# Performance work log

Measured on AMD Instinct MI355X. Metric: run time of the kernel, lower is better.

Reference implementation:

```python
import jax, jax.numpy as jnp
import numpy as np

B, T, H = 65536, 34, 64
T10_LO, T10_HI = 0.1, 5.0
M0_LO, M0_HI = 0.0, 10000.0


def setup_inputs() -> dict:
    key = jax.random.key(0)
    ks = jax.random.split(key, 24)
    sig = jax.random.uniform(ks[0], (B, T), jnp.float32, 0.1, 1.0)
    keep = jax.random.uniform(ks[1], (B, T)) > 0.3
    X_fa_in = jnp.where(keep, sig, 0.0)
    fa_vals = jax.random.uniform(ks[2], (B, T), jnp.float32, 0.05, 0.6)  # flip angles (rad)
    fa_mask = keep
    fa_len = jnp.sum(keep, axis=1).astype(jnp.int64)
    TR_vals = jax.random.uniform(ks[3], (B, 1), jnp.float32, 0.003, 0.01)
    gi = 1.0 / np.sqrt(H)
    p = {}
    p['gru_Wih'] = jax.random.uniform(ks[4], (3 * H, 2), jnp.float32, -gi, gi)
    p['gru_Whh'] = jax.random.uniform(ks[5], (3 * H, H), jnp.float32, -gi, gi)
    p['gru_bih'] = jax.random.uniform(ks[6], (3 * H,), jnp.float32, -gi, gi)
    p['gru_bhh'] = jax.random.uniform(ks[7], (3 * H,), jnp.float32, -gi, gi)
    p['score_T10_w'] = jax.random.normal(ks[8], (H,), jnp.float32) * gi
    p['score_M0_w'] = jax.random.normal(ks[9], (H,), jnp.float32) * gi
    def lin(kw, kb, fan_out, fan_in):
        b = 1.0 / np.sqrt(fan_in)
        return (jax.random.uniform(kw, (fan_out, fan_in), jnp.float32, -b, b),
                jax.random.uniform(kb, (fan_out,), jnp.float32, -b, b))
    p['regT_W1'], p['regT_b1'] = lin(ks[10], ks[11], 200, H)
    p['regT_W2'], p['regT_b2'] = lin(ks[12], ks[13], 200, 200)
    p['regT_W3'], p['regT_b3'] = lin(ks[14], ks[15], 1, 200)
    p['regM_W1'], p['regM_b1'] = lin(ks[16], ks[17], 200, H)
    p['regM_W2'], p['regM_b2'] = lin(ks[18], ks[19], 200, 200)
    p['regM_W3'], p['regM_b3'] = lin(ks[20], ks[21], 1, 200)
    return dict(X_fa_in=X_fa_in, fa_vals=fa_vals, fa_mask=fa_mask, fa_len=fa_len,
                TR_vals=TR_vals, **p)


def _forward_fill(X_fa_in, fa_vals):
    # Segmented last-observation-carried-forward via cummax of valid indices.
    valid = X_fa_in != 0
    idx = jnp.where(valid, jnp.arange(T)[None, :], -1)
    last = jax.lax.cummax(idx, axis=1)                     # [B,T] index of last nonzero
    g = jnp.clip(last, 0, T - 1)
    Xf = jnp.where(last >= 0, jnp.take_along_axis(X_fa_in, g, axis=1), 0.0)
    ff = jnp.where(last >= 0, jnp.take_along_axis(fa_vals, g, axis=1), 0.0)
    return Xf, ff


def _gru(x, Wih, Whh, bih, bhh):
    # x: [B,T,2] -> out: [B,T,H]; PyTorch GRU gate order (r, z, n)
    x_proj = jnp.einsum('btf,gf->btg', x, Wih) + bih       # [B,T,3H]
    def step(h, xp):
        gh = h @ Whh.T + bhh                               # [B,3H]
        xr, xz, xn = jnp.split(xp, 3, axis=-1)
        hr, hz, hn = jnp.split(gh, 3, axis=-1)
        r = jax.nn.sigmoid(xr + hr)
        z = jax.nn.sigmoid(xz + hz)
        n = jnp.tanh(xn + r * hn)
        h_new = (1.0 - z) * n + z * h
        return h_new, h_new
    h0 = jnp.zeros((x.shape[0], Whh.shape[1]), x.dtype)
    _, out = jax.lax.scan(step, h0, jnp.swapaxes(x_proj, 0, 1))
    return jnp.swapaxes(out, 0, 1)


def _mlp(h, W1, b1, W2, b2, W3, b3):
    # Dropout layers are identity in eval mode
    h = jax.nn.elu(h @ W1.T + b1)
    h = jax.nn.elu(h @ W2.T + b2)
    return h @ W3.T + b3


def reference(X_fa_in, fa_vals, fa_mask, fa_len, TR_vals,
              gru_Wih, gru_Whh, gru_bih, gru_bhh,
              score_T10_w, score_M0_w,
              regT_W1, regT_b1, regT_W2, regT_b2, regT_W3, regT_b3,
              regM_W1, regM_b1, regM_W2, regM_b2, regM_W3, regM_b3):
    Xf, ff = _forward_fill(X_fa_in, fa_vals)
    x = jnp.stack([Xf, ff], axis=-1)                       # [B,T,2]
    out = _gru(x, gru_Wih, gru_Whh, gru_bih, gru_bhh)      # [B,T,H]
    # attention pooling: softmax over time of a linear score
    sT = jax.nn.softmax(out @ score_T10_w, axis=1)[..., None]
    sM = jax.nn.softmax(out @ score_M0_w, axis=1)[..., None]
    hT = jnp.sum(out * sT, axis=1)                         # [B,H]
    hM = jnp.sum(out * sM, axis=1)
    T10_raw = _mlp(hT, regT_W1, regT_b1, regT_W2, regT_b2, regT_W3, regT_b3)[:, 0]
    M0_raw = _mlp(hM, regM_W1, regM_b1, regM_W2, regM_b2, regM_W3, regM_b3)[:, 0]
    T10 = T10_LO + jax.nn.sigmoid(T10_raw)[:, None] * (T10_HI - T10_LO)  # [B,1]
    M0 = M0_LO + jax.nn.sigmoid(M0_raw)[:, None] * (M0_HI - M0_LO)       # [B,1]
    R1 = 1.0 / T10
    E = jnp.exp(-TR_vals * R1)                             # [B,1]
    X_out = (1.0 - E) * jnp.sin(fa_vals) / (1.0 - jnp.cos(fa_vals) * E)  # [B,T]
    X_out = X_out * M0
    return (X_out, T10, M0)
```

## Files before the change

### kernel.cpp

```cpp
#include <hip/hip_runtime.h>

#define B_TOT 65536
#define T_LEN 34
#define HD 64
#define LOG2E 1.44269504088896340736f

typedef __attribute__((ext_vector_type(8))) short short8b;
typedef __attribute__((ext_vector_type(4))) short short4b;
typedef __attribute__((ext_vector_type(4))) float f32x4;
typedef __attribute__((ext_vector_type(4))) unsigned int u32x4;

__device__ __forceinline__ float frcp(float x){ return __builtin_amdgcn_rcpf(x); }
__device__ __forceinline__ float fexp2(float x){ return __builtin_amdgcn_exp2f(x); }
__device__ __forceinline__ float fsigmoid(float x){ return frcp(1.0f+__expf(-x)); }
__device__ __forceinline__ float felu(float x){ return x>0.0f ? x : (__expf(x)-1.0f); }

__device__ __forceinline__ unsigned short f2bf_rne(float f){
    unsigned int u = __float_as_uint(f);
    u += 0x7FFFu + ((u >> 16) & 1u);
    return (unsigned short)(u >> 16);
}
__device__ __forceinline__ float bf2f(unsigned short h){
    return __uint_as_float(((unsigned int)h) << 16);
}
__device__ __forceinline__ void split8(const float4& a, const float4& b,
                                       short8b& hi, short8b& lo){
    float f[8] = {a.x,a.y,a.z,a.w,b.x,b.y,b.z,b.w};
    #pragma unroll
    for (int i = 0; i < 8; ++i){
        unsigned short h = f2bf_rne(f[i]);
        hi[i] = (short)h;
        lo[i] = (short)f2bf_rne(f[i] - bf2f(h));
    }
}
__device__ __forceinline__ unsigned int cvt_pk_bf16(float lo, float hi){
    unsigned int r;
    asm("v_cvt_pk_bf16_f32 %0, %1, %2" : "=v"(r) : "v"(lo), "v"(hi));
    return r;
}
__device__ __forceinline__ int hswz(int r){ return ((r ^ (r >> 3)) & 7); }

__global__ __launch_bounds__(256)
void gru_attn_mfma(const float* __restrict__ Xin, const float* __restrict__ FA,
                   const float* __restrict__ Wih, const float* __restrict__ Whh,
                   const float* __restrict__ bih, const float* __restrict__ bhh,
                   const float* __restrict__ swT, const float* __restrict__ swM,
                   float* __restrict__ hT_out, float* __restrict__ hM_out)
{
    __shared__ __align__(16) unsigned short WF[28*512];
    __shared__ __align__(16) unsigned short HL[4][1024];
    __shared__ unsigned int XF[T_LEN*64];
    __shared__ __align__(8)  unsigned short XWc[12][16][4];

    const int tid  = threadIdx.x;
    const int lane = tid & 63;
    const int wv   = tid >> 6;
    const int l16  = lane & 15;
    const int lhi  = lane >> 4;

    for (int f = wv; f < 28; f += 4) {
        unsigned short* dst = &WF[f*512 + lane*8];
        if (f < 24) {
            int ks = f / 12, nt = f % 12;
            int u_out = nt*16 + l16;
            float scale = (nt < 8) ? -LOG2E : 2.0f*LOG2E;
            #pragma unroll
            for (int j = 0; j < 8; ++j) {
                int k = ks*32 + lhi*8 + j;
                int u_in = (k & 3)*16 + (k >> 2);
                dst[j] = f2bf_rne(scale*Whh[u_out*64 + u_in]);
            }
        } else {
            int s = f - 24;
            const float* src = (s >= 2) ? swM : swT;
            int ks = s & 1;
            #pragma unroll
            for (int j = 0; j < 8; ++j) {
                int k = ks*32 + lhi*8 + j;
                int u_in = (k & 3)*16 + (k >> 2);
                dst[j] = f2bf_rne(LOG2E*src[u_in]);
            }
        }
    }
    if (tid < 192) {
        int nt  = tid >> 4;
        int u16 = tid & 15;
        int u_abs = (nt < 8) ? (nt*16 + u16) : (128 + (nt-8)*16 + u16);
        float s = (nt < 8) ? -LOG2E : 2.0f*LOG2E;
        float bias = (nt < 8) ? -LOG2E*(bih[u_abs] + bhh[u_abs])
                              : 2.0f*LOG2E*bih[u_abs];
        XWc[nt][u16][0] = f2bf_rne(s*Wih[u_abs*2]);
        XWc[nt][u16][1] = f2bf_rne(s*Wih[u_abs*2+1]);
        XWc[nt][u16][2] = f2bf_rne(bias);
        XWc[nt][u16][3] = 0;
    }

    #pragma unroll
    for (int i = 0; i < 16; ++i) HL[wv][i*64 + lane] = 0;

    const int rowbase = blockIdx.x*64 + wv*16;

    for (int rr = 0; rr < 16; ++rr) {
        int row = rowbase + rr;
        float X = 0.0f, fa = 0.0f; int idx = -1;
        if (lane < T_LEN) {
            X  = Xin[row*T_LEN + lane];
            fa = FA [row*T_LEN + lane];
            if (X != 0.0f) idx = lane;
        }
        #pragma unroll
        for (int off = 1; off < 64; off <<= 1) {
            int v = __shfl_up(idx, off);
            if (lane >= off && v > idx) idx = v;
        }
        int gsrc = idx < 0 ? 0 : idx;
        float Xg = __shfl(X,  gsrc);
        float fg = __shfl(fa, gsrc);
        if (idx < 0) { Xg = 0.0f; fg = 0.0f; }
        if (lane < T_LEN)
            XF[lane*64 + wv*16 + rr] =
                (unsigned int)f2bf_rne(Xg) | ((unsigned int)f2bf_rne(fg) << 16);
    }

    float biasN[4];
    #pragma unroll
    for (int g = 0; g < 4; ++g) biasN[g] = 2.0f*LOG2E*bhh[128 + g*16 + l16];

    __syncthreads();

    const int sA    = hswz(l16) << 3;
    const int aoff0 = l16*64 + (( lhi   *8) ^ sA);
    const int aoff1 = l16*64 + (((4+lhi)*8) ^ sA);
    const int xfidx = wv*16 + l16;
    const unsigned int extk2 = (lhi == 0) ? 0x00003f80u : 0u;
    const bool ext0 = (lhi == 0);
    const f32x4 zero4 = (f32x4){0.f, 0.f, 0.f, 0.f};

    float2 hreg2[4][2];
    float2 numT2[4][2], numM2[4][2];
    float  denT[4] = {}, denM[4] = {};
    #pragma unroll
    for (int q = 0; q < 4; ++q)
        #pragma unroll
        for (int j = 0; j < 2; ++j) {
            hreg2[q][j] = make_float2(0.f, 0.f);
            numT2[q][j] = make_float2(0.f, 0.f);
            numM2[q][j] = make_float2(0.f, 0.f);
        }

    const unsigned short* HLr = HL[wv];
    unsigned short*       HLw = HL[wv];
    const unsigned short* WFl = &WF[lane*8];
    const uint2*          XWp = reinterpret_cast<const uint2*>(&XWc[0][0][0]);

    for (int t = 0; t < T_LEN; ++t) {
        short8b a0 = *reinterpret_cast<const short8b*>(&HLr[aoff0]);
        short8b a1 = *reinterpret_cast<const short8b*>(&HLr[aoff1]);
        unsigned int xw = XF[t*64 + xfidx];
        u32x4 aeu = { ext0 ? xw : 0u, extk2, 0u, 0u };
        short8b aext = __builtin_bit_cast(short8b, aeu);

        f32x4 accT = __builtin_amdgcn_mfma_f32_16x16x32_bf16(
            a0, *reinterpret_cast<const short8b*>(WFl + 24*512), zero4, 0,0,0);
        accT = __builtin_amdgcn_mfma_f32_16x16x32_bf16(
            a1, *reinterpret_cast<const short8b*>(WFl + 25*512), accT, 0,0,0);
        f32x4 accM = __builtin_amdgcn_mfma_f32_16x16x32_bf16(
            a0, *reinterpret_cast<const short8b*>(WFl + 26*512), zero4, 0,0,0);
        accM = __builtin_amdgcn_mfma_f32_16x16x32_bf16(
            a1, *reinterpret_cast<const short8b*>(WFl + 27*512), accM, 0,0,0);

        if (t) {
            #pragma unroll
            for (int q = 0; q < 4; ++q) {
                float eT = fexp2(accT[q]);
                float eM = fexp2(accM[q]);
                denT[q] += eT; denM[q] += eM;
                #pragma unroll
                for (int j = 0; j < 2; ++j) {
                    numT2[q][j].x = fmaf(eT, hreg2[q][j].x, numT2[q][j].x);
                    numT2[q][j].y = fmaf(eT, hreg2[q][j].y, numT2[q][j].y);
                    numM2[q][j].x = fmaf(eM, hreg2[q][j].x, numM2[q][j].x);
                    numM2[q][j].y = fmaf(eM, hreg2[q][j].y, numM2[q][j].y);
                }
            }
        }

        #pragma unroll
        for (int g = 0; g < 4; ++g) {
            uint2 er = XWp[(g   )*16 + l16];
            uint2 ez = XWp[(4+g )*16 + l16];
            uint2 en = XWp[(8+g )*16 + l16];
            u32x4 bru = { ext0 ? er.x : 0u, ext0 ? er.y : 0u, 0u, 0u };
            u32x4 bzu = { ext0 ? ez.x : 0u, ext0 ? ez.y : 0u, 0u, 0u };
            u32x4 bnu = { ext0 ? en.x : 0u, ext0 ? en.y : 0u, 0u, 0u };

            f32x4 ar = __builtin_amdgcn_mfma_f32_16x16x32_bf16(
                aext, __builtin_bit_cast(short8b, bru), zero4, 0,0,0);
            ar = __builtin_amdgcn_mfma_f32_16x16x32_bf16(
                a0, *reinterpret_cast<const short8b*>(WFl + (g   )*512), ar, 0,0,0);
            ar = __builtin_amdgcn_mfma_f32_16x16x32_bf16(
                a1, *reinterpret_cast<const short8b*>(WFl + (12+g)*512), ar, 0,0,0);
            f32x4 az = __builtin_amdgcn_mfma_f32_16x16x32_bf16(
                aext, __builtin_bit_cast(short8b, bzu), zero4, 0,0,0);
            az = __builtin_amdgcn_mfma_f32_16x16x32_bf16(
                a0, *reinterpret_cast<const short8b*>(WFl + (4+g )*512), az, 0,0,0);
            az = __builtin_amdgcn_mfma_f32_16x16x32_bf16(
                a1, *reinterpret_cast<const short8b*>(WFl + (16+g)*512), az, 0,0,0);
            f32x4 anx = __builtin_amdgcn_mfma_f32_16x16x32_bf16(
                aext, __builtin_bit_cast(short8b, bnu), zero4, 0,0,0);
            f32x4 anh = __builtin_amdgcn_mfma_f32_16x16x32_bf16(
                a0, *reinterpret_cast<const short8b*>(WFl + (8+g )*512), zero4, 0,0,0);
            anh = __builtin_amdgcn_mfma_f32_16x16x32_bf16(
                a1, *reinterpret_cast<const short8b*>(WFl + (20+g)*512), anh, 0,0,0);
            #pragma unroll
            for (int q = 0; q < 4; ++q) {
                float r  = frcp(1.0f + fexp2(ar[q]));
                float z  = frcp(1.0f + fexp2(az[q]));
                float v  = fmaf(r, anh[q], fmaf(r, biasN[g], anx[q]));
                float n  = fmaf(-2.0f, frcp(1.0f + fexp2(v)), 1.0f);
                float h  = (g & 1) ? hreg2[q][g>>1].y : hreg2[q][g>>1].x;
                float hn = fmaf(z, h - n, n);
                if (g & 1) hreg2[q][g>>1].y = hn; else hreg2[q][g>>1].x = hn;
            }
        }

        #pragma unroll
        for (int q = 0; q < 4; ++q) {
            int rloc = lhi*4 + q;
            unsigned int d0 = cvt_pk_bf16(hreg2[q][0].x, hreg2[q][0].y);
            unsigned int d1 = cvt_pk_bf16(hreg2[q][1].x, hreg2[q][1].y);
            int so = rloc*64 + ((l16*4) ^ (hswz(rloc) << 3));
            *reinterpret_cast<uint2*>(&HLw[so]) = make_uint2(d0, d1);
        }
    }

    {
        short8b a0 = *reinterpret_cast<const short8b*>(&HLr[aoff0]);
        short8b a1 = *reinterpret_cast<const short8b*>(&HLr[aoff1]);
        f32x4 accT = __builtin_amdgcn_mfma_f32_16x16x32_bf16(
            a0, *reinterpret_cast<const short8b*>(WFl + 24*512), zero4, 0,0,0);
        accT = __builtin_amdgcn_mfma_f32_16x16x32_bf16(
            a1, *reinterpret_cast<const short8b*>(WFl + 25*512), accT, 0,0,0);
        f32x4 accM = __builtin_amdgcn_mfma_f32_16x16x32_bf16(
            a0, *reinterpret_cast<const short8b*>(WFl + 26*512), zero4, 0,0,0);
        accM = __builtin_amdgcn_mfma_f32_16x16x32_bf16(
            a1, *reinterpret_cast<const short8b*>(WFl + 27*512), accM, 0,0,0);
        #pragma unroll
        for (int q = 0; q < 4; ++q) {
            float eT = fexp2(accT[q]);
            float eM = fexp2(accM[q]);
            denT[q] += eT; denM[q] += eM;
            #pragma unroll
            for (int j = 0; j < 2; ++j) {
                numT2[q][j].x = fmaf(eT, hreg2[q][j].x, numT2[q][j].x);
                numT2[q][j].y = fmaf(eT, hreg2[q][j].y, numT2[q][j].y);
                numM2[q][j].x = fmaf(eM, hreg2[q][j].x, numM2[q][j].x);
                numM2[q][j].y = fmaf(eM, hreg2[q][j].y, numM2[q][j].y);
            }
        }
    }

    #pragma unroll
    for (int q = 0; q < 4; ++q) {
        int row = rowbase + lhi*4 + q;
        float rT = frcp(denT[q]), rM = frcp(denM[q]);
        #pragma unroll
        for (int j = 0; j < 2; ++j) {
            hT_out[row*HD + (2*j  )*16 + l16] = numT2[q][j].x*rT;
            hT_out[row*HD + (2*j+1)*16 + l16] = numT2[q][j].y*rT;
            hM_out[row*HD + (2*j  )*16 + l16] = numM2[q][j].x*rM;
            hM_out[row*HD + (2*j+1)*16 + l16] = numM2[q][j].y*rM;
        }
    }
}

__global__ __launch_bounds__(256)
void mlp_mfma(const float* __restrict__ hT, const float* __restrict__ hM,
    const float* __restrict__ TW1, const float* __restrict__ Tb1,
    const float* __restrict__ TW2, const float* __restrict__ Tb2,
    const float* __restrict__ TW3, const float* __restrict__ Tb3,
    const float* __restrict__ MW1, const float* __restrict__ Mb1,
    const float* __restrict__ MW2, const float* __restrict__ Mb2,
    const float* __restrict__ MW3, const float* __restrict__ Mb3,
    const float* __restrict__ FA, const float* __restrict__ TR,
    float* __restrict__ out)
{
    __shared__ __align__(16) unsigned short xh[2*64*64];
    __shared__ __align__(16) unsigned short h1s[64*256];
    __shared__ float praw[4][64];
    __shared__ float rawv[2][64];
    __shared__ float Es[64], M0s[64];

    const int tid  = threadIdx.x;
    const int lane = tid & 63;
    const int wv   = tid >> 6;
    const int l16  = lane & 15;
    const int lhi  = lane >> 4;
    const int row0 = blockIdx.x*64;

    {
        int r  = tid >> 2;
        int k0 = (tid & 3) * 16;
        int rx = r & 7;
        const float* pT = &hT[(row0+r)*64 + k0];
        const float* pM = &hM[(row0+r)*64 + k0];
        #pragma unroll
        for (int j = 0; j < 4; ++j) {
            float4 vT = *reinterpret_cast<const float4*>(pT + 4*j);
            float4 vM = *reinterpret_cast<const float4*>(pM + 4*j);
            int kk = k0 + 4*j;
            int ad = r*64 + ((((kk>>3) ^ rx))<<3) + (kk&7);
            short4b sT = { (short)f2bf_rne(vT.x), (short)f2bf_rne(vT.y),
                           (short)f2bf_rne(vT.z), (short)f2bf_rne(vT.w) };
            short4b sM = { (short)f2bf_rne(vM.x), (short)f2bf_rne(vM.y),
                           (short)f2bf_rne(vM.z), (short)f2bf_rne(vM.w) };
            *reinterpret_cast<short4b*>(&xh[ad])        = sT;
            *reinterpret_cast<short4b*>(&xh[4096 + ad]) = sM;
        }
        for (int i = tid; i < 64*24; i += 256) {
            int rr = i / 24, kk = 200 + i % 24;
            h1s[rr*256 + ((((kk>>3) ^ (rr&7)))<<3) + (kk&7)] = 0;
        }
    }
    __syncthreads();

    for (int brn = 0; brn < 2; ++brn) {
        const float* W1 = brn ? MW1 : TW1; const float* b1 = brn ? Mb1 : Tb1;
        const float* W2 = brn ? MW2 : TW2; const float* b2 = brn ? Mb2 : Tb2;
        const float* W3 = brn ? MW3 : TW3; const float* b3 = brn ? Mb3 : Tb3;

        for (int s = 0; s < 4; ++s) {
            int nt = wv + 4*s;
            if (nt > 12) break;
            int n  = nt*16 + l16;
            int nc = n < 200 ? n : 199;
            float bv = b1[nc];
            f32x4 acc[4];
            #pragma unroll
            for (int mt = 0; mt < 4; ++mt) acc[mt] = (f32x4){bv,bv,bv,bv};
            #pragma unroll
            for (int ks = 0; ks < 2; ++ks) {
                int k0 = ks*32 + lhi*8;
                const float* wp = &W1[nc*64 + k0];
                float4 w0 = *reinterpret_cast<const float4*>(wp);
                float4 w1 = *reinterpret_cast<const float4*>(wp + 4);
                short8b bh, bl;
                split8(w0, w1, bh, bl);
                #pragma unroll
                for (int mt = 0; mt < 4; ++mt) {
                    int rr = mt*16 + l16;
                    short8b a = *reinterpret_cast<const short8b*>(
                        &xh[brn*4096 + rr*64 + ((((k0>>3) ^ (rr&7)))<<3)]);
                    acc[mt] = __builtin_amdgcn_mfma_f32_16x16x32_bf16(a, bh, acc[mt], 0,0,0);
                    acc[mt] = __builtin_amdgcn_mfma_f32_16x16x32_bf16(a, bl, acc[mt], 0,0,0);
                }
            }
            if (n < 200) {
                #pragma unroll
                for (int mt = 0; mt < 4; ++mt) {
                    #pragma unroll
                    for (int q = 0; q < 4; ++q) {
                        int rr = mt*16 + lhi*4 + q;
                        h1s[rr*256 + ((((n>>3) ^ (rr&7)))<<3) + (n&7)] =
                            f2bf_rne(felu(acc[mt][q]));
                    }
                }
            }
        }
        __syncthreads();

        float p[4][4] = {};
        for (int s = 0; s < 4; ++s) {
            int nt = wv + 4*s;
            if (nt > 12) break;
            int n  = nt*16 + l16;
            int nc = n < 200 ? n : 199;
            float w3v = (n < 200) ? W3[nc] : 0.0f;
            float bv = b2[nc];
            f32x4 acc[4];
            #pragma unroll
            for (int mt = 0; mt < 4; ++mt) acc[mt] = (f32x4){bv,bv,bv,bv};
            for (int ks = 0; ks < 7; ++ks) {
                int k0 = ks*32 + lhi*8;
                short8b bh, bl;
                if (k0 + 8 <= 200) {
                    const float* wp = &W2[nc*200 + k0];
                    float4 w0 = *reinterpret_cast<const float4*>(wp);
                    float4 w1 = *reinterpret_cast<const float4*>(wp + 4);
                    split8(w0, w1, bh, bl);
                } else {
                    #pragma unroll
                    for (int i = 0; i < 8; ++i) { bh[i] = 0; bl[i] = 0; }
                }
                #pragma unroll
                for (int mt = 0; mt < 4; ++mt) {
                    int rr = mt*16 + l16;
                    short8b a = *reinterpret_cast<const short8b*>(
                        &h1s[rr*256 + ((((k0>>3) ^ (rr&7)))<<3)]);
                    acc[mt] = __builtin_amdgcn_mfma_f32_16x16x32_bf16(a, bh, acc[mt], 0,0,0);
                    acc[mt] = __builtin_amdgcn_mfma_f32_16x16x32_bf16(a, bl, acc[mt], 0,0,0);
                }
            }
            #pragma unroll
            for (int mt = 0; mt < 4; ++mt)
                #pragma unroll
                for (int q = 0; q < 4; ++q)
                    p[mt][q] = fmaf(w3v, felu(acc[mt][q]), p[mt][q]);
        }
        #pragma unroll
        for (int off = 1; off < 16; off <<= 1) {
            #pragma unroll
            for (int mt = 0; mt < 4; ++mt)
                #pragma unroll
                for (int q = 0; q < 4; ++q)
                    p[mt][q] += __shfl_xor(p[mt][q], off);
        }
        if (l16 == 0) {
            #pragma unroll
            for (int mt = 0; mt < 4; ++mt)
                #pragma unroll
                for (int q = 0; q < 4; ++q)
                    praw[wv][mt*16 + lhi*4 + q] = p[mt][q];
        }
        __syncthreads();
        if (tid < 64)
            rawv[brn][tid] = b3[0] + praw[0][tid] + praw[1][tid] + praw[2][tid] + praw[3][tid];
        __syncthreads();
    }

    if (tid < 64) {
        int row = row0 + tid;
        float T10 = 0.1f + 4.9f*fsigmoid(rawv[0][tid]);
        float M0  = 10000.0f*fsigmoid(rawv[1][tid]);
        Es[tid]  = __expf(-TR[row]/T10);
        M0s[tid] = M0;
        out[(size_t)B_TOT*T_LEN + row]         = T10;
        out[(size_t)B_TOT*T_LEN + B_TOT + row] = M0;
    }
    __syncthreads();
    for (int i = tid; i < 64*T_LEN; i += 256) {
        int rr = i / T_LEN, t = i - rr*T_LEN;
        int row = row0 + rr;
        float fa = FA[row*T_LEN + t];
        float s = __sinf(fa), c = __cosf(fa);
        float Ev = Es[rr];
        out[row*T_LEN + t] = (1.0f - Ev)*s*frcp(1.0f - c*Ev)*M0s[rr];
    }
}

extern "C" void kernel_launch(void* const* d_in, const int* in_sizes, int n_in,
                              void* d_out, int out_size, void* d_ws, size_t ws_size,
                              hipStream_t stream) {
    const float* Xin = (const float*)d_in[0];
    const float* FA  = (const float*)d_in[1];
    const float* TR  = (const float*)d_in[4];
    const float* Wih = (const float*)d_in[5];
    const float* Whh = (const float*)d_in[6];
    const float* bih = (const float*)d_in[7];
    const float* bhh = (const float*)d_in[8];
    const float* swT = (const float*)d_in[9];
    const float* swM = (const float*)d_in[10];
    const float* TW1 = (const float*)d_in[11]; const float* Tb1 = (const float*)d_in[12];
    const float* TW2 = (const float*)d_in[13]; const float* Tb2 = (const float*)d_in[14];
    const float* TW3 = (const float*)d_in[15]; const float* Tb3 = (const float*)d_in[16];
    const float* MW1 = (const float*)d_in[17]; const float* Mb1 = (const float*)d_in[18];
    const float* MW2 = (const float*)d_in[19]; const float* Mb2 = (const float*)d_in[20];
    const float* MW3 = (const float*)d_in[21]; const float* Mb3 = (const float*)d_in[22];
    float* out = (float*)d_out;

    float* hT = (float*)d_ws;
    float* hM = hT + (size_t)B_TOT*HD;

    gru_attn_mfma<<<B_TOT/64, 256, 0, stream>>>(Xin, FA, Wih, Whh, bih, bhh,
                                                swT, swM, hT, hM);
    mlp_mfma<<<B_TOT/64, 256, 0, stream>>>(hT, hM,
                                           TW1, Tb1, TW2, Tb2, TW3, Tb3,
                                           MW1, Mb1, MW2, Mb2, MW3, Mb3,
                                           FA, TR, out);
}
```

Before: 283.0 us.

## Split GRU recurrence and attention pooling into separate producer/consumer warps

```diff
diff --git a/kernel.cpp b/kernel.cpp
--- a/kernel.cpp
+++ b/kernel.cpp
@@ -40,7 +40,7 @@
 }
 __device__ __forceinline__ int hswz(int r){ return ((r ^ (r >> 3)) & 7); }
 
-__global__ __launch_bounds__(256)
+__global__ __launch_bounds__(512)
 void gru_attn_mfma(const float* __restrict__ Xin, const float* __restrict__ FA,
                    const float* __restrict__ Wih, const float* __restrict__ Whh,
                    const float* __restrict__ bih, const float* __restrict__ bhh,
@@ -48,7 +48,7 @@
                    float* __restrict__ hT_out, float* __restrict__ hM_out)
 {
     __shared__ __align__(16) unsigned short WF[28*512];
-    __shared__ __align__(16) unsigned short HL[4][1024];
+    __shared__ __align__(16) unsigned short HL[4][2][1024];
     __shared__ unsigned int XF[T_LEN*64];
     __shared__ __align__(8)  unsigned short XWc[12][16][4];
 
@@ -57,8 +57,10 @@
     const int wv   = tid >> 6;
     const int l16  = lane & 15;
     const int lhi  = lane >> 4;
-
-    for (int f = wv; f < 28; f += 4) {
+    const int wgru = wv & 3;
+    const bool isPool = (wv >= 4);
+
+    for (int f = wv; f < 28; f += 8) {
         unsigned short* dst = &WF[f*512 + lane*8];
         if (f < 24) {
             int ks = f / 12, nt = f % 12;
@@ -94,14 +96,12 @@
         XWc[nt][u16][2] = f2bf_rne(bias);
         XWc[nt][u16][3] = 0;
     }
-
-    #pragma unroll
-    for (int i = 0; i < 16; ++i) HL[wv][i*64 + lane] = 0;
-
-    const int rowbase = blockIdx.x*64 + wv*16;
-
-    for (int rr = 0; rr < 16; ++rr) {
-        int row = rowbase + rr;
+    for (int i = tid; i < 4*2*1024; i += 512)
+        (&HL[0][0][0])[i] = 0;
+
+    for (int i = 0; i < 8; ++i) {
+        int brow = wv*8 + i;
+        int row  = blockIdx.x*64 + brow;
         float X = 0.0f, fa = 0.0f; int idx = -1;
         if (lane < T_LEN) {
             X  = Xin[row*T_LEN + lane];
@@ -118,158 +118,184 @@
         float fg = __shfl(fa, gsrc);
         if (idx < 0) { Xg = 0.0f; fg = 0.0f; }
         if (lane < T_LEN)
-            XF[lane*64 + wv*16 + rr] =
+            XF[lane*64 + brow] =
                 (unsigned int)f2bf_rne(Xg) | ((unsigned int)f2bf_rne(fg) << 16);
     }
-
-    float biasN[4];
-    #pragma unroll
-    for (int g = 0; g < 4; ++g) biasN[g] = 2.0f*LOG2E*bhh[128 + g*16 + l16];
 
     __syncthreads();
 
     const int sA    = hswz(l16) << 3;
     const int aoff0 = l16*64 + (( lhi   *8) ^ sA);
     const int aoff1 = l16*64 + (((4+lhi)*8) ^ sA);
-    const int xfidx = wv*16 + l16;
-    const unsigned int extk2 = (lhi == 0) ? 0x00003f80u : 0u;
-    const bool ext0 = (lhi == 0);
     const f32x4 zero4 = (f32x4){0.f, 0.f, 0.f, 0.f};
-
-    float2 hreg2[4][2];
-    float2 numT2[4][2], numM2[4][2];
-    float  denT[4] = {}, denM[4] = {};
-    #pragma unroll
-    for (int q = 0; q < 4; ++q)
-        #pragma unroll
-        for (int j = 0; j < 2; ++j) {
-            hreg2[q][j] = make_float2(0.f, 0.f);
-            numT2[q][j] = make_float2(0.f, 0.f);
-            numM2[q][j] = make_float2(0.f, 0.f);
-        }
-
-    const unsigned short* HLr = HL[wv];
-    unsigned short*       HLw = HL[wv];
     const unsigned short* WFl = &WF[lane*8];
-    const uint2*          XWp = reinterpret_cast<const uint2*>(&XWc[0][0][0]);
-
-    for (int t = 0; t < T_LEN; ++t) {
-        short8b a0 = *reinterpret_cast<const short8b*>(&HLr[aoff0]);
-        short8b a1 = *reinterpret_cast<const short8b*>(&HLr[aoff1]);
-        unsigned int xw = XF[t*64 + xfidx];
-        u32x4 aeu = { ext0 ? xw : 0u, extk2, 0u, 0u };
-        short8b aext = __builtin_bit_cast(short8b, aeu);
-
-        f32x4 accT = __builtin_amdgcn_mfma_f32_16x16x32_bf16(
-            a0, *reinterpret_cast<const short8b*>(WFl + 24*512), zero4, 0,0,0);
-        accT = __builtin_amdgcn_mfma_f32_16x16x32_bf16(
-            a1, *reinterpret_cast<const short8b*>(WFl + 25*512), accT, 0,0,0);
-        f32x4 accM = __builtin_amdgcn_mfma_f32_16x16x32_bf16(
-            a0, *reinterpret_cast<const short8b*>(WFl + 26*512), zero4, 0,0,0);
-        accM = __builtin_amdgcn_mfma_f32_16x16x32_bf16(
-            a1, *reinterpret_cast<const short8b*>(WFl + 27*512), accM, 0,0,0);
-
-        if (t) {
+
+    if (!isPool) {
+        __builtin_amdgcn_s_setprio(1);
+        const unsigned int extk2 = (lhi == 0) ? 0x00003f80u : 0u;
+        const bool ext0 = (lhi == 0);
+        const uint2* XWp = reinterpret_cast<const uint2*>(&XWc[0][0][0]);
+        float biasN[4];
+        #pragma unroll
+        for (int g = 0; g < 4; ++g) biasN[g] = 2.0f*LOG2E*bhh[128 + g*16 + l16];
+
+        float2 hreg2[4][2];
+        #pragma unroll
+        for (int q = 0; q < 4; ++q) { hreg2[q][0] = make_float2(0.f,0.f);
+                                      hreg2[q][1] = make_float2(0.f,0.f); }
+
+        for (int t = 0; t < T_LEN; ++t) {
+            __syncthreads();
+            const unsigned short* pb = &HL[wgru][(t+1)&1][0];
+            unsigned short*       cb = &HL[wgru][ t   &1][0];
+            short8b a0 = *reinterpret_cast<const short8b*>(&pb[aoff0]);
+            short8b a1 = *reinterpret_cast<const short8b*>(&pb[aoff1]);
+            unsigned int xw = XF[t*64 + wgru*16 + l16];
+            u32x4 aeu = { ext0 ? xw : 0u, extk2, 0u, 0u };
+            short8b aext = __builtin_bit_cast(short8b, aeu);
+
+            #pragma unroll
+            for (int g = 0; g < 4; ++g) {
+                uint2 er = XWp[(g   )*16 + l16];
+                uint2 ez = XWp[(4+g )*16 + l16];
+                uint2 en = XWp[(8+g )*16 + l16];
+                u32x4 bru = { ext0 ? er.x : 0u, ext0 ? er.y : 0u, 0u, 0u };
+                u32x4 bzu = { ext0 ? ez.x : 0u, ext0 ? ez.y : 0u, 0u, 0u };
+                u32x4 bnu = { ext0 ? en.x : 0u, ext0 ? en.y : 0u, 0u, 0u };
+
+                f32x4 ar = __builtin_amdgcn_mfma_f32_16x16x32_bf16(
+                    aext, __builtin_bit_cast(short8b, bru), zero4, 0,0,0);
+                ar = __builtin_amdgcn_mfma_f32_16x16x32_bf16(
+                    a0, *reinterpret_cast<const short8b*>(WFl + (g   )*512), ar, 0,0,0);
+                ar = __builtin_amdgcn_mfma_f32_16x16x32_bf16(
+                    a1, *reinterpret_cast<const short8b*>(WFl + (12+g)*512), ar, 0,0,0);
+                f32x4 az = __builtin_amdgcn_mfma_f32_16x16x32_bf16(
+                    aext, __builtin_bit_cast(short8b, bzu), zero4, 0,0,0);
+                az = __builtin_amdgcn_mfma_f32_16x16x32_bf16(
+                    a0, *reinterpret_cast<const short8b*>(WFl + (4+g )*512), az, 0,0,0);
+                az = __builtin_amdgcn_mfma_f32_16x16x32_bf16(
+                    a1, *reinterpret_cast<const short8b*>(WFl + (16+g)*512), az, 0,0,0);
+                f32x4 anx = __builtin_amdgcn_mfma_f32_16x16x32_bf16(
+                    aext, __builtin_bit_cast(short8b, bnu), zero4, 0,0,0);
+                f32x4 anh = __builtin_amdgcn_mfma_f32_16x16x32_bf16(
+                    a0, *reinterpret_cast<const short8b*>(WFl + (8+g )*512), zero4, 0,0,0);
+                anh = __builtin_amdgcn_mfma_f32_16x16x32_bf16(
+                    a1, *reinterpret_cast<const short8b*>(WFl + (20+g)*512), anh, 0,0,0);
+                #pragma unroll
+                for (int q = 0; q < 4; ++q) {
+                    float r  = frcp(1.0f + fexp2(ar[q]));
+                    float z  = frcp(1.0f + fexp2(az[q]));
+                    float v  = fmaf(r, anh[q], fmaf(r, biasN[g], anx[q]));
+                    float n  = fmaf(-2.0f, frcp(1.0f + fexp2(v)), 1.0f);
+                    float h  = (g & 1) ? hreg2[q][g>>1].y : hreg2[q][g>>1].x;
+                    float hn = fmaf(z, h - n, n);
+                    if (g & 1) hreg2[q][g>>1].y = hn; else hreg2[q][g>>1].x = hn;
+                }
+            }
             #pragma unroll
             for (int q = 0; q < 4; ++q) {
+                int rloc = lhi*4 + q;
+                unsigned int d0 = cvt_pk_bf16(hreg2[q][0].x, hreg2[q][0].y);
+                unsigned int d1 = cvt_pk_bf16(hreg2[q][1].x, hreg2[q][1].y);
+                int so = rloc*64 + ((l16*4) ^ (hswz(rloc) << 3));
+                *reinterpret_cast<uint2*>(&cb[so]) = make_uint2(d0, d1);
+            }
+        }
+        __syncthreads();
+    } else {
+        float2 numT2[4][2], numM2[4][2];
+        float  denT[4] = {}, denM[4] = {};
+        #pragma unroll
+        for (int q = 0; q < 4; ++q)
+            #pragma unroll
+            for (int j = 0; j < 2; ++j) {
+                numT2[q][j] = make_float2(0.f, 0.f);
+                numM2[q][j] = make_float2(0.f, 0.f);
+            }
+
+        for (int t = 0; t < T_LEN; ++t) {
+            __syncthreads();
+            if (t == 0) continue;
+            const unsigned short* pb = &HL[wgru][(t+1)&1][0];
+            short8b a0 = *reinterpret_cast<const short8b*>(&pb[aoff0]);
+            short8b a1 = *reinterpret_cast<const short8b*>(&pb[aoff1]);
+            f32x4 accT = __builtin_amdgcn_mfma_f32_16x16x32_bf16(
+                a0, *reinterpret_cast<const short8b*>(WFl + 24*512), zero4, 0,0,0);
+            accT = __builtin_amdgcn_mfma_f32_16x16x32_bf16(
+                a1, *reinterpret_cast<const short8b*>(WFl + 25*512), accT, 0,0,0);
+            f32x4 accM = __builtin_amdgcn_mfma_f32_16x16x32_bf16(
+                a0, *reinterpret_cast<const short8b*>(WFl + 26*512), zero4, 0,0,0);
+            accM = __builtin_amdgcn_mfma_f32_16x16x32_bf16(
+                a1, *reinterpret_cast<const short8b*>(WFl + 27*512), accM, 0,0,0);
+            #pragma unroll
+            for (int q = 0; q < 4; ++q) {
+                int rloc = lhi*4 + q;
+                uint2 hq = *reinterpret_cast<const uint2*>(
+                    &pb[rloc*64 + ((l16*4) ^ (hswz(rloc) << 3))]);
+                float g0 = __uint_as_float(hq.x << 16);
+                float g1 = __uint_as_float(hq.x & 0xFFFF0000u);
+                float g2 = __uint_as_float(hq.y << 16);
+                float g3 = __uint_as_float(hq.y & 0xFFFF0000u);
                 float eT = fexp2(accT[q]);
                 float eM = fexp2(accM[q]);
                 denT[q] += eT; denM[q] += eM;
-                #pragma unroll
-                for (int j = 0; j < 2; ++j) {
-                    numT2[q][j].x = fmaf(eT, hreg2[q][j].x, numT2[q][j].x);
-                    numT2[q][j].y = fmaf(eT, hreg2[q][j].y, numT2[q][j].y);
-                    numM2[q][j].x = fmaf(eM, hreg2[q][j].x, numM2[q][j].x);
-                    numM2[q][j].y = fmaf(eM, hreg2[q][j].y, numM2[q][j].y);
-                }
-            }
-        }
-
-        #pragma unroll
-        for (int g = 0; g < 4; ++g) {
-            uint2 er = XWp[(g   )*16 + l16];
-            uint2 ez = XWp[(4+g )*16 + l16];
-            uint2 en = XWp[(8+g )*16 + l16];
-            u32x4 bru = { ext0 ? er.x : 0u, ext0 ? er.y : 0u, 0u, 0u };
-            u32x4 bzu = { ext0 ? ez.x : 0u, ext0 ? ez.y : 0u, 0u, 0u };
-            u32x4 bnu = { ext0 ? en.x : 0u, ext0 ? en.y : 0u, 0u, 0u };
-
-            f32x4 ar = __builtin_amdgcn_mfma_f32_16x16x32_bf16(
-                aext, __builtin_bit_cast(short8b, bru), zero4, 0,0,0);
-            ar = __builtin_amdgcn_mfma_f32_16x16x32_bf16(
-                a0, *reinterpret_cast<const short8b*>(WFl + (g   )*512), ar, 0,0,0);
-            ar = __builtin_amdgcn_mfma_f32_16x16x32_bf16(
-                a1, *reinterpret_cast<const short8b*>(WFl + (12+g)*512), ar, 0,0,0);
-            f32x4 az = __builtin_amdgcn_mfma_f32_16x16x32_bf16(
-                aext, __builtin_bit_cast(short8b, bzu), zero4, 0,0,0);
-            az = __builtin_amdgcn_mfma_f32_16x16x32_bf16(
-                a0, *reinterpret_cast<const short8b*>(WFl + (4+g )*512), az, 0,0,0);
-            az = __builtin_amdgcn_mfma_f32_16x16x32_bf16(
-                a1, *reinterpret_cast<const short8b*>(WFl + (16+g)*512), az, 0,0,0);
-            f32x4 anx = __builtin_amdgcn_mfma_f32_16x16x32_bf16(
-                aext, __builtin_bit_cast(short8b, bnu), zero4, 0,0,0);
-            f32x4 anh = __builtin_amdgcn_mfma_f32_16x16x32_bf16(
-                a0, *reinterpret_cast<const short8b*>(WFl + (8+g )*512), zero4, 0,0,0);
-            anh = __builtin_amdgcn_mfma_f32_16x16x32_bf16(
-                a1, *reinterpret_cast<const short8b*>(WFl + (20+g)*512), anh, 0,0,0);
+                numT2[q][0].x = fmaf(eT, g0, numT2[q][0].x);
+                numT2[q][0].y = fmaf(eT, g1, numT2[q][0].y);
+                numT2[q][1].x = fmaf(eT, g2, numT2[q][1].x);
+                numT2[q][1].y = fmaf(eT, g3, numT2[q][1].y);
+                numM2[q][0].x = fmaf(eM, g0, numM2[q][0].x);
+                numM2[q][0].y = fmaf(eM, g1, numM2[q][0].y);
+                numM2[q][1].x = fmaf(eM, g2, numM2[q][1].x);
+                numM2[q][1].y = fmaf(eM, g3, numM2[q][1].y);
+            }
+        }
+        __syncthreads();
+        {
+            const unsigned short* pb = &HL[wgru][1][0];
+            short8b a0 = *reinterpret_cast<const short8b*>(&pb[aoff0]);
+            short8b a1 = *reinterpret_cast<const short8b*>(&pb[aoff1]);
+            f32x4 accT = __builtin_amdgcn_mfma_f32_16x16x32_bf16(
+                a0, *reinterpret_cast<const short8b*>(WFl + 24*512), zero4, 0,0,0);
+            accT = __builtin_amdgcn_mfma_f32_16x16x32_bf16(
+                a1, *reinterpret_cast<const short8b*>(WFl + 25*512), accT, 0,0,0);
+            f32x4 accM = __builtin_amdgcn_mfma_f32_16x16x32_bf16(
+                a0, *reinterpret_cast<const short8b*>(WFl + 26*512), zero4, 0,0,0);
+            accM = __builtin_amdgcn_mfma_f32_16x16x32_bf16(
+                a1, *reinterpret_cast<const short8b*>(WFl + 27*512), accM, 0,0,0);
             #pragma unroll
             for (int q = 0; q < 4; ++q) {
-                float r  = frcp(1.0f + fexp2(ar[q]));
-                float z  = frcp(1.0f + fexp2(az[q]));
-                float v  = fmaf(r, anh[q], fmaf(r, biasN[g], anx[q]));
-                float n  = fmaf(-2.0f, frcp(1.0f + fexp2(v)), 1.0f);
-                float h  = (g & 1) ? hreg2[q][g>>1].y : hreg2[q][g>>1].x;
-                float hn = fmaf(z, h - n, n);
-                if (g & 1) hreg2[q][g>>1].y = hn; else hreg2[q][g>>1].x = hn;
-            }
-        }
-
+                int rloc = lhi*4 + q;
+                uint2 hq = *reinterpret_cast<const uint2*>(
+                    &pb[rloc*64 + ((l16*4) ^ (hswz(rloc) << 3))]);
+                float g0 = __uint_as_float(hq.x << 16);
+                float g1 = __uint_as_float(hq.x & 0xFFFF0000u);
+                float g2 = __uint_as_float(hq.y << 16);
+                float g3 = __uint_as_float(hq.y & 0xFFFF0000u);
+                float eT = fexp2(accT[q]);
+                float eM = fexp2(accM[q]);
+                denT[q] += eT; denM[q] += eM;
+                numT2[q][0].x = fmaf(eT, g0, numT2[q][0].x);
+                numT2[q][0].y = fmaf(eT, g1, numT2[q][0].y);
+                numT2[q][1].x = fmaf(eT, g2, numT2[q][1].x);
+                numT2[q][1].y = fmaf(eT, g3, numT2[q][1].y);
+                numM2[q][0].x = fmaf(eM, g0, numM2[q][0].x);
+                numM2[q][0].y = fmaf(eM, g1, numM2[q][0].y);
+                numM2[q][1].x = fmaf(eM, g2, numM2[q][1].x);
+                numM2[q][1].y = fmaf(eM, g3, numM2[q][1].y);
+            }
+        }
+        const int rowbase = blockIdx.x*64 + wgru*16;
         #pragma unroll
         for (int q = 0; q < 4; ++q) {
-            int rloc = lhi*4 + q;
-            unsigned int d0 = cvt_pk_bf16(hreg2[q][0].x, hreg2[q][0].y);
-            unsigned int d1 = cvt_pk_bf16(hreg2[q][1].x, hreg2[q][1].y);
-            int so = rloc*64 + ((l16*4) ^ (hswz(rloc) << 3));
-            *reinterpret_cast<uint2*>(&HLw[so]) = make_uint2(d0, d1);
-        }
-    }
-
-    {
-        short8b a0 = *reinterpret_cast<const short8b*>(&HLr[aoff0]);
-        short8b a1 = *reinterpret_cast<const short8b*>(&HLr[aoff1]);
-        f32x4 accT = __builtin_amdgcn_mfma_f32_16x16x32_bf16(
-            a0, *reinterpret_cast<const short8b*>(WFl + 24*512), zero4, 0,0,0);
-        accT = __builtin_amdgcn_mfma_f32_16x16x32_bf16(
-            a1, *reinterpret_cast<const short8b*>(WFl + 25*512), accT, 0,0,0);
-        f32x4 accM = __builtin_amdgcn_mfma_f32_16x16x32_bf16(
-            a0, *reinterpret_cast<const short8b*>(WFl + 26*512), zero4, 0,0,0);
-        accM = __builtin_amdgcn_mfma_f32_16x16x32_bf16(
-            a1, *reinterpret_cast<const short8b*>(WFl + 27*512), accM, 0,0,0);
-        #pragma unroll
-        for (int q = 0; q < 4; ++q) {
-            float eT = fexp2(accT[q]);
-            float eM = fexp2(accM[q]);
-            denT[q] += eT; denM[q] += eM;
+            int row = rowbase + lhi*4 + q;
+            float rT = frcp(denT[q]), rM = frcp(denM[q]);
             #pragma unroll
             for (int j = 0; j < 2; ++j) {
-                numT2[q][j].x = fmaf(eT, hreg2[q][j].x, numT2[q][j].x);
-                numT2[q][j].y = fmaf(eT, hreg2[q][j].y, numT2[q][j].y);
-                numM2[q][j].x = fmaf(eM, hreg2[q][j].x, numM2[q][j].x);
-                numM2[q][j].y = fmaf(eM, hreg2[q][j].y, numM2[q][j].y);
-            }
-        }
-    }
-
-    #pragma unroll
-    for (int q = 0; q < 4; ++q) {
-        int row = rowbase + lhi*4 + q;
-        float rT = frcp(denT[q]), rM = frcp(denM[q]);
-        #pragma unroll
-        for (int j = 0; j < 2; ++j) {
-            hT_out[row*HD + (2*j  )*16 + l16] = numT2[q][j].x*rT;
-            hT_out[row*HD + (2*j+1)*16 + l16] = numT2[q][j].y*rT;
-            hM_out[row*HD + (2*j  )*16 + l16] = numM2[q][j].x*rM;
-            hM_out[row*HD + (2*j+1)*16 + l16] = numM2[q][j].y*rM;
+                hT_out[row*HD + (2*j  )*16 + l16] = numT2[q][j].x*rT;
+                hT_out[row*HD + (2*j+1)*16 + l16] = numT2[q][j].y*rT;
+                hM_out[row*HD + (2*j  )*16 + l16] = numM2[q][j].x*rM;
+                hM_out[row*HD + (2*j+1)*16 + l16] = numM2[q][j].y*rM;
+            }
         }
     }
 }
@@ -471,7 +497,7 @@
     float* hT = (float*)d_ws;
     float* hM = hT + (size_t)B_TOT*HD;
 
-    gru_attn_mfma<<<B_TOT/64, 256, 0, stream>>>(Xin, FA, Wih, Whh, bih, bhh,
+    gru_attn_mfma<<<B_TOT/64, 512, 0, stream>>>(Xin, FA, Wih, Whh, bih, bhh,
                                                 swT, swM, hT, hM);
     mlp_mfma<<<B_TOT/64, 256, 0, stream>>>(hT, hM,
                                            TW1, Tb1, TW2, Tb2, TW3, Tb3,
```

Result: faster. 239.5 us (-15.4%).
